# Kernel tuning notes

Hardware: AMD Instinct MI355X
Metric: run time of the kernel (lower is better)

The kernel has to match this reference:

```python
import jax, jax.numpy as jnp
import numpy as np
from jax import lax

B, L, LQ, D_IN, ET, H, INIT_EMBED = 16, 256, 64, 32, 128, 4, 8
DIM = 2 * D_IN          # attention value/feature dim (x concat mask)
ETK = ET // H           # per-head time-embedding dim


def _lin(key, fan_in, shape):
    b = 1.0 / np.sqrt(fan_in)
    return jax.random.uniform(key, shape, jnp.float32, -b, b)


def setup_inputs() -> dict:
    key = jax.random.key(0)
    ks = jax.random.split(key, 24)
    inp = {
        "x": jax.random.normal(ks[0], (B, L, D_IN), jnp.float32),
        "time_steps": jnp.sort(jax.random.uniform(ks[1], (B, L), jnp.float32), axis=-1),
        "mask": (jax.random.uniform(ks[2], (B, L, D_IN)) > 0.5).astype(jnp.float32),
        "query": jnp.linspace(0.0, 1.0, LQ, dtype=jnp.float32),
        # time embedding: Linear(1,1) and Linear(1, ET-1)
        "w_lin": _lin(ks[3], 1, (1,)), "b_lin": _lin(ks[4], 1, (1,)),
        "w_per": _lin(ks[5], 1, (ET - 1,)), "b_per": _lin(ks[6], 1, (ET - 1,)),
        # attention projections (stored as (in,out))
        "Wq": _lin(ks[7], ET, (ET, ET)), "bq": _lin(ks[8], ET, (ET,)),
        "Wk": _lin(ks[9], ET, (ET, ET)), "bk": _lin(ks[10], ET, (ET,)),
        "Wo": _lin(ks[11], H * DIM, (H * DIM, ET)), "bo": _lin(ks[12], H * DIM, (ET,)),
        # vanilla RNN (tanh)
        "W_ih": _lin(ks[13], ET, (ET, ET)), "b_ih": _lin(ks[14], ET, (ET,)),
        "W_hh": _lin(ks[15], ET, (ET, ET)), "b_hh": _lin(ks[16], ET, (ET,)),
        "r1_w": _lin(ks[17], ET, (ET, 128)), "r1_b": _lin(ks[17], ET, (128,)),
        "r2_w": _lin(ks[18], 128, (128, 128)), "r2_b": _lin(ks[18], 128, (128,)),
        "r3_w": _lin(ks[19], 128, (128, ET)), "r3_b": _lin(ks[19], 128, (ET,)),
        "r4_w": _lin(ks[20], ET, (ET, INIT_EMBED)), "r4_b": _lin(ks[20], ET, (INIT_EMBED,)),
    }
    return inp


def reference(x, time_steps, mask, query,
              w_lin, b_lin, w_per, b_per,
              Wq, bq, Wk, bk, Wo, bo,
              W_ih, b_ih, W_hh, b_hh,
              r1_w, r1_b, r2_w, r2_b, r3_w, r3_b, r4_w, r4_b):
    def time_embed(tt):  # (...,) -> (..., ET)
        tt = tt[..., None]
        return jnp.concatenate([tt * w_lin + b_lin,
                                jnp.sin(tt * w_per + b_per)], axis=-1)

    xc = jnp.concatenate([x, mask], axis=-1)          # (B,L,DIM) value
    m2 = jnp.concatenate([mask, mask], axis=-1)       # (B,L,DIM)

    kemb = time_embed(time_steps)                     # (B,L,ET)
    qemb = time_embed(query)                          # (LQ,ET)

    q = (qemb @ Wq + bq).reshape(LQ, H, ETK).transpose(1, 0, 2)       # (H,LQ,ETK)
    k = (kemb @ Wk + bk).reshape(B, L, H, ETK).transpose(0, 2, 1, 3)  # (B,H,L,ETK)

    scores = jnp.einsum('hqe,bhke->bhqk', q, k) / np.sqrt(ETK)        # (B,H,LQ,L)
    # per-feature mask broadcast: (B,H,LQ,L,DIM)
    s5 = jnp.where(m2[:, None, None, :, :] == 0, -1e9, scores[..., None])
    p = jax.nn.softmax(s5, axis=-2)                   # softmax over keys L
    att = jnp.einsum('bhqkd,bkd->bhqd', p, xc)        # (B,H,LQ,DIM)
    att = att.transpose(0, 2, 1, 3).reshape(B, LQ, H * DIM)
    out = att @ Wo + bo                               # (B,LQ,ET)

    # vanilla tanh RNN, return final hidden state
    def step(h, xt):
        h = jnp.tanh(xt @ W_ih + b_ih + h @ W_hh + b_hh)
        return h, None
    h0 = jnp.zeros((B, ET), out.dtype)
    hT, _ = lax.scan(step, h0, out.transpose(1, 0, 2))  # scan over LQ

    y = hT @ r1_w + r1_b
    y = y @ r2_w + r2_b
    y = y @ r3_w + r3_b
    y = y @ r4_w + r4_b                               # (B, INIT_EMBED)
    return y
```

## Files before the change

### kernel.cpp

```cpp
#include <hip/hip_runtime.h>
#include <hip/hip_bf16.h>


#define NB 16
#define NL 256
#define NLQ 64
#define NDIN 32
#define NET 128
#define NH 4
#define NETK 32

#define HPAD 136
#define PAD(i) ((i) + 4 * ((i) >> 6))

#define ESS 20
#define ORP 132

__global__ __launch_bounds__(128) void k_embed_proj(
    const float* __restrict__ ts, const float* __restrict__ query,
    const float* __restrict__ w_lin, const float* __restrict__ b_lin,
    const float* __restrict__ w_per, const float* __restrict__ b_per,
    const float* __restrict__ Wk, const float* __restrict__ bk,
    const float* __restrict__ Wq, const float* __restrict__ bq,
    float* __restrict__ kproj, float* __restrict__ qproj) {
  __shared__ float emb[8 * NET];
  int g = blockIdx.x;
  int j = threadIdx.x;
  bool isQ = (g >= 512);
  int base = (isQ ? g - 512 : g) * 8;
  float wl_ = w_lin[0], bl_ = b_lin[0];
  float wp = (j > 0) ? w_per[j - 1] : 0.f;
  float bp = (j > 0) ? b_per[j - 1] : 0.f;
#pragma unroll
  for (int rr = 0; rr < 8; rr++) {
    float t = isQ ? query[base + rr] : ts[base + rr];
    emb[rr * NET + j] = (j == 0) ? (t * wl_ + bl_) : sinf(t * wp + bp);
  }
  __syncthreads();
  const float* W = isQ ? Wq : Wk;
  float bias = isQ ? bq[j] : bk[j];
  float acc[8];
#pragma unroll
  for (int rr = 0; rr < 8; rr++) acc[rr] = bias;
#pragma unroll 4
  for (int i = 0; i < NET; i++) {
    float wv = W[i * NET + j];
#pragma unroll
    for (int rr = 0; rr < 8; rr++) acc[rr] += emb[rr * NET + i] * wv;
  }
  float* dst = isQ ? qproj : kproj;
#pragma unroll
  for (int rr = 0; rr < 8; rr++) dst[(size_t)(base + rr) * NET + j] = acc[rr];
}

__global__ __launch_bounds__(256) void k_attn_fused(
    const float* __restrict__ x, const float* __restrict__ mask,
    const float* __restrict__ qproj, const float* __restrict__ kproj,
    const float* __restrict__ Wo, const float* __restrict__ bo,
    const float* __restrict__ Wih, const float* __restrict__ bih,
    const float* __restrict__ bhh, float* __restrict__ XW) {
  const float SC = 0.17677669529663687f;
  int blk = blockIdx.x;
  int qg = blk & 15;
  int b  = blk >> 4;
  int t  = threadIdx.x;

  __shared__ float xs[NL * NDIN];
  __shared__ unsigned mb[NL];
  __shared__ float es[NL * ESS];
  __shared__ float qs[4 * NET];
  __shared__ float arow[4 * 256];
  __shared__ float orow[4 * ORP];

  {
    int qq = t >> 7;
    int e  = t & 127;
    qs[qq * NET + e]       = qproj[(size_t)(qg * 4 + qq) * NET + e];
    qs[(qq + 2) * NET + e] = qproj[(size_t)(qg * 4 + qq + 2) * NET + e];
  }
  {
    const float4* src = (const float4*)(x + (size_t)b * NL * NDIN);
    float4* dst = (float4*)xs;
#pragma unroll
    for (int u = 0; u < 8; u++) dst[t + 256 * u] = src[t + 256 * u];
  }
  {
    const float4* mr4 = (const float4*)(mask + (size_t)(b * NL + t) * NDIN);
    unsigned bits = 0;
#pragma unroll
    for (int u = 0; u < 8; u++) {
      float4 m = mr4[u];
      bits |= (m.x != 0.f ? 1u : 0u) << (4 * u);
      bits |= (m.y != 0.f ? 1u : 0u) << (4 * u + 1);
      bits |= (m.z != 0.f ? 1u : 0u) << (4 * u + 2);
      bits |= (m.w != 0.f ? 1u : 0u) << (4 * u + 3);
    }
    mb[t] = bits;
  }
  __syncthreads();

  for (int h = 0; h < NH; h++) {
    float kr[NETK];
    const float4* kp =
        (const float4*)(kproj + (size_t)(b * NL + t) * NET + h * NETK);
#pragma unroll
    for (int i = 0; i < 8; i++) {
      float4 v = kp[i];
      kr[4 * i] = v.x; kr[4 * i + 1] = v.y;
      kr[4 * i + 2] = v.z; kr[4 * i + 3] = v.w;
    }
#pragma unroll
    for (int qq = 0; qq < 4; qq++) {
      const float* qv = &qs[qq * NET + h * NETK];
      float s0 = 0.f, s1 = 0.f;
#pragma unroll
      for (int i = 0; i < NETK; i += 2) {
        s0 += qv[i] * kr[i];
        s1 += qv[i + 1] * kr[i + 1];
      }
      es[t * ESS + qq * 4 + h] = __expf((s0 + s1) * SC);
    }
  }
  __syncthreads();

  {
    int s = t & 1;
    int p = t >> 1;
    int qq = p >> 5;
    int c  = p & 31;
    int k0 = s * 128;
    float den[NH] = {0.f, 0.f, 0.f, 0.f};
    float num[NH] = {0.f, 0.f, 0.f, 0.f};
    float sumx = 0.f;
#pragma unroll 4
    for (int k = k0; k < k0 + 128; k++) {
      float xv = xs[k * NDIN + c];
      float mv = ((mb[k] >> c) & 1u) ? 1.f : 0.f;
      float4 e4 = *(const float4*)(es + k * ESS + qq * 4);
      sumx += xv;
      float e0 = e4.x * mv, e1 = e4.y * mv, e2 = e4.z * mv, e3 = e4.w * mv;
      den[0] += e0; num[0] += e0 * xv;
      den[1] += e1; num[1] += e1 * xv;
      den[2] += e2; num[2] += e2 * xv;
      den[3] += e3; num[3] += e3 * xv;
    }
    sumx += __shfl_xor(sumx, 1, 64);
#pragma unroll
    for (int h = 0; h < NH; h++) {
      den[h] += __shfl_xor(den[h], 1, 64);
      num[h] += __shfl_xor(num[h], 1, 64);
    }
    if (s == 0) {
      float meanx = sumx * (1.f / 256.f);
#pragma unroll
      for (int h = 0; h < NH; h++) {
        bool any = (den[h] > 0.f);
        arow[qq * 256 + h * 64 + c]      = any ? (num[h] / den[h]) : meanx;
        arow[qq * 256 + h * 64 + 32 + c] = any ? 1.f : 0.f;
      }
    }
  }
  __syncthreads();

  {
    int j = t & 127;
    int half = t >> 7;
    float o0 = bo[j], o1 = o0;
#pragma unroll 4
    for (int u = 0; u < 256; u++) {
      float w = Wo[(size_t)u * NET + j];
      o0 += arow[half * 256 + u] * w;
      o1 += arow[(half + 2) * 256 + u] * w;
    }
    orow[half * ORP + j] = o0;
    orow[(half + 2) * ORP + j] = o1;
  }
  __syncthreads();

  {
    int j = t & 127;
    int half = t >> 7;
    float a0 = bih[j] + bhh[j], a1 = a0;
#pragma unroll 4
    for (int e = 0; e < NET; e++) {
      float w = Wih[(size_t)e * NET + j];
      a0 += orow[half * ORP + e] * w;
      a1 += orow[(half + 2) * ORP + e] * w;
    }
    int q0 = qg * 4 + half;
    XW[(size_t)(b * NLQ + q0) * NET + j]     = a0;
    XW[(size_t)(b * NLQ + q0 + 2) * NET + j] = a1;
  }
}

__device__ __forceinline__ void layer128(const float* src_lds,
                                         const float* __restrict__ W,
                                         const float* __restrict__ bvec,
                                         float* dst_lds, int j, int s) {
  const float4* h4 = (const float4*)(src_lds + s * 68);
  float a0 = 0.f, a1 = 0.f, a2 = 0.f, a3 = 0.f;
#pragma unroll
  for (int i = 0; i < 16; i++) {
    float4 hv = h4[i];
    int base = (s * 64 + 4 * i) * NET + j;
    a0 += hv.x * W[base];
    a1 += hv.y * W[base + NET];
    a2 += hv.z * W[base + 2 * NET];
    a3 += hv.w * W[base + 3 * NET];
  }
  float acc = (a0 + a1) + (a2 + a3);
  acc += __shfl_xor(acc, 1, 64);
  if (s == 0) dst_lds[PAD(j)] = acc + bvec[j];
}

__global__ __launch_bounds__(256, 1) void k_rnn(
    const float* __restrict__ XW, const float* __restrict__ Whh,
    const float* __restrict__ r1w, const float* __restrict__ r1b,
    const float* __restrict__ r2w, const float* __restrict__ r2b,
    const float* __restrict__ r3w, const float* __restrict__ r3b,
    const float* __restrict__ r4w, const float* __restrict__ r4b,
    float* __restrict__ out) {
  int b = blockIdx.x;
  int tid = threadIdx.x;
  int s = tid & 1;
  int j = tid >> 1;
  __shared__ float xwl[NLQ * NET];
  __shared__ float hb[2][HPAD];
  __shared__ float tmp[HPAD];

  {
    const float4* src = (const float4*)(XW + (size_t)b * NLQ * NET);
    float4* dst = (float4*)xwl;
#pragma unroll
    for (int u = 0; u < 8; u++) dst[tid + 256 * u] = src[tid + 256 * u];
  }
  float w[64];
#pragma unroll
  for (int i = 0; i < 64; i++) w[i] = Whh[(s * 64 + i) * NET + j];

  if (tid < 128) hb[0][PAD(tid)] = 0.f;
  __syncthreads();

  for (int t = 0; t < NLQ; t++) {
    float xwv = xwl[t * NET + j];
    const float4* h4 = (const float4*)&hb[t & 1][s * 68];
    float a0 = 0.f, a1 = 0.f, a2 = 0.f, a3 = 0.f;
#pragma unroll
    for (int i = 0; i < 16; i++) {
      float4 hv = h4[i];
      a0 += hv.x * w[4 * i];
      a1 += hv.y * w[4 * i + 1];
      a2 += hv.z * w[4 * i + 2];
      a3 += hv.w * w[4 * i + 3];
    }
    float acc = (a0 + a1) + (a2 + a3);
    acc += __shfl_xor(acc, 1, 64);
    if (s == 0) {
      float z = acc + xwv;
      float e2 = __expf(2.f * z);
      hb[(t + 1) & 1][PAD(j)] = 1.f - 2.f / (e2 + 1.f);
    }
    __syncthreads();
  }

  layer128(hb[0], r1w, r1b, tmp, j, s);
  __syncthreads();
  layer128(tmp, r2w, r2b, hb[1], j, s);
  __syncthreads();
  layer128(hb[1], r3w, r3b, hb[0], j, s);
  __syncthreads();
  if (tid < 64) {
    int jj = tid >> 3, p = tid & 7;
    float y = 0.f;
#pragma unroll
    for (int i = 0; i < 16; i++) {
      int ii = p * 16 + i;
      y += hb[0][PAD(ii)] * r4w[ii * 8 + jj];
    }
    y += __shfl_xor(y, 1, 64);
    y += __shfl_xor(y, 2, 64);
    y += __shfl_xor(y, 4, 64);
    if (p == 0) out[b * 8 + jj] = y + r4b[jj];
  }
}

extern "C" void kernel_launch(void* const* d_in, const int* in_sizes, int n_in,
                              void* d_out, int out_size, void* d_ws, size_t ws_size,
                              hipStream_t stream) {
  const float* x     = (const float*)d_in[0];
  const float* ts    = (const float*)d_in[1];
  const float* mask  = (const float*)d_in[2];
  const float* query = (const float*)d_in[3];
  const float* w_lin = (const float*)d_in[4];
  const float* b_lin = (const float*)d_in[5];
  const float* w_per = (const float*)d_in[6];
  const float* b_per = (const float*)d_in[7];
  const float* Wq    = (const float*)d_in[8];
  const float* bq    = (const float*)d_in[9];
  const float* Wk    = (const float*)d_in[10];
  const float* bk    = (const float*)d_in[11];
  const float* Wo    = (const float*)d_in[12];
  const float* bo    = (const float*)d_in[13];
  const float* Wih   = (const float*)d_in[14];
  const float* bih   = (const float*)d_in[15];
  const float* Whh   = (const float*)d_in[16];
  const float* bhh   = (const float*)d_in[17];
  const float* r1w   = (const float*)d_in[18];
  const float* r1b   = (const float*)d_in[19];
  const float* r2w   = (const float*)d_in[20];
  const float* r2b   = (const float*)d_in[21];
  const float* r3w   = (const float*)d_in[22];
  const float* r3b   = (const float*)d_in[23];
  const float* r4w   = (const float*)d_in[24];
  const float* r4b   = (const float*)d_in[25];
  float* out = (float*)d_out;

  float* ws    = (float*)d_ws;
  float* kproj = ws;
  float* qproj = ws + 524288;
  float* XW    = ws + 532480;

  k_embed_proj<<<520, 128, 0, stream>>>(
      ts, query, w_lin, b_lin, w_per, b_per, Wk, bk, Wq, bq, kproj, qproj);
  k_attn_fused<<<NB * 16, 256, 0, stream>>>(
      x, mask, qproj, kproj, Wo, bo, Wih, bih, bhh, XW);
  k_rnn<<<NB, 256, 0, stream>>>(XW, Whh, r1w, r1b, r2w, r2b, r3w, r3b,
                                r4w, r4b, out);
}
```

Baseline: 195.2 us.

## Double attention block to 512 threads with split-key reduction and rotated score layout

The fused attention kernel now runs 512 threads per block instead of 256. Each thread computes scores for two heads of one key, reading q straight from global memory rather than staging it in LDS. The weighted-sum pass is split across two key halves with a partial-sum exchange through LDS. Score storage uses a rotated column layout to reduce LDS bank conflicts, and the Wo/Wih projections are given one query row per thread. This adds parallelism and more threads in flight, at the cost of extra barriers and higher register pressure from the 64-element key array.

```diff
diff --git a/kernel.cpp b/kernel.cpp
--- a/kernel.cpp
+++ b/kernel.cpp
@@ -53,7 +53,7 @@
   for (int rr = 0; rr < 8; rr++) dst[(size_t)(base + rr) * NET + j] = acc[rr];
 }
 
-__global__ __launch_bounds__(256) void k_attn_fused(
+__global__ __launch_bounds__(512, 2) void k_attn_fused(
     const float* __restrict__ x, const float* __restrict__ mask,
     const float* __restrict__ qproj, const float* __restrict__ kproj,
     const float* __restrict__ Wo, const float* __restrict__ bo,
@@ -65,26 +65,20 @@
   int b  = blk >> 4;
   int t  = threadIdx.x;
 
-  __shared__ float xs[NL * NDIN];
+  __shared__ __align__(16) float xs[NL * NDIN];
   __shared__ unsigned mb[NL];
-  __shared__ float es[NL * ESS];
-  __shared__ float qs[4 * NET];
+  __shared__ __align__(16) float es[NL * ESS];
   __shared__ float arow[4 * 256];
   __shared__ float orow[4 * ORP];
-
-  {
-    int qq = t >> 7;
-    int e  = t & 127;
-    qs[qq * NET + e]       = qproj[(size_t)(qg * 4 + qq) * NET + e];
-    qs[(qq + 2) * NET + e] = qproj[(size_t)(qg * 4 + qq + 2) * NET + e];
-  }
+  float* part = es;
+
   {
     const float4* src = (const float4*)(x + (size_t)b * NL * NDIN);
     float4* dst = (float4*)xs;
 #pragma unroll
-    for (int u = 0; u < 8; u++) dst[t + 256 * u] = src[t + 256 * u];
-  }
-  {
+    for (int u = 0; u < 4; u++) dst[t + 512 * u] = src[t + 512 * u];
+  }
+  if (t < NL) {
     const float4* mr4 = (const float4*)(mask + (size_t)(b * NL + t) * NDIN);
     unsigned bits = 0;
 #pragma unroll
@@ -99,44 +93,52 @@
   }
   __syncthreads();
 
-  for (int h = 0; h < NH; h++) {
-    float kr[NETK];
+  {
+    int k  = t & 255;
+    int hp = t >> 8;
+    float kr[64];
     const float4* kp =
-        (const float4*)(kproj + (size_t)(b * NL + t) * NET + h * NETK);
-#pragma unroll
-    for (int i = 0; i < 8; i++) {
+        (const float4*)(kproj + (size_t)(b * NL + k) * NET + hp * 64);
+#pragma unroll
+    for (int i = 0; i < 16; i++) {
       float4 v = kp[i];
       kr[4 * i] = v.x; kr[4 * i + 1] = v.y;
       kr[4 * i + 2] = v.z; kr[4 * i + 3] = v.w;
     }
+    int rot = (k >> 3) & 3;
 #pragma unroll
     for (int qq = 0; qq < 4; qq++) {
-      const float* qv = &qs[qq * NET + h * NETK];
+      const float* qrow = qproj + (size_t)(qg * 4 + qq) * NET + hp * 64;
       float s0 = 0.f, s1 = 0.f;
 #pragma unroll
-      for (int i = 0; i < NETK; i += 2) {
-        s0 += qv[i] * kr[i];
-        s1 += qv[i + 1] * kr[i + 1];
+      for (int i = 0; i < 32; i++) {
+        s0 += qrow[i] * kr[i];
+        s1 += qrow[32 + i] * kr[32 + i];
       }
-      es[t * ESS + qq * 4 + h] = __expf((s0 + s1) * SC);
-    }
-  }
-  __syncthreads();
-
-  {
-    int s = t & 1;
-    int p = t >> 1;
-    int qq = p >> 5;
-    int c  = p & 31;
-    int k0 = s * 128;
-    float den[NH] = {0.f, 0.f, 0.f, 0.f};
-    float num[NH] = {0.f, 0.f, 0.f, 0.f};
-    float sumx = 0.f;
+      float2 ev = make_float2(__expf(s0 * SC), __expf(s1 * SC));
+      int col = ((qq + rot) & 3) * 4 + hp * 2;
+      *(float2*)&es[k * ESS + col] = ev;
+    }
+  }
+  __syncthreads();
+
+  float den[NH], num[NH], sumx;
+  int qq, c, s, kh;
+  {
+    int w = t >> 6, lane = t & 63;
+    qq = w & 3; kh = w >> 2;
+    s = lane & 1; c = lane >> 1;
+    int k0 = kh * 128 + s * 64;
+#pragma unroll
+    for (int h = 0; h < NH; h++) { den[h] = 0.f; num[h] = 0.f; }
+    sumx = 0.f;
 #pragma unroll 4
-    for (int k = k0; k < k0 + 128; k++) {
+    for (int kk = 0; kk < 64; kk++) {
+      int k = k0 + kk;
       float xv = xs[k * NDIN + c];
       float mv = ((mb[k] >> c) & 1u) ? 1.f : 0.f;
-      float4 e4 = *(const float4*)(es + k * ESS + qq * 4);
+      int col = ((qq + ((k >> 3) & 3)) & 3) * 4;
+      float4 e4 = *(const float4*)(es + k * ESS + col);
       sumx += xv;
       float e0 = e4.x * mv, e1 = e4.y * mv, e2 = e4.z * mv, e3 = e4.w * mv;
       den[0] += e0; num[0] += e0 * xv;
@@ -150,46 +152,50 @@
       den[h] += __shfl_xor(den[h], 1, 64);
       num[h] += __shfl_xor(num[h], 1, 64);
     }
-    if (s == 0) {
-      float meanx = sumx * (1.f / 256.f);
-#pragma unroll
-      for (int h = 0; h < NH; h++) {
-        bool any = (den[h] > 0.f);
-        arow[qq * 256 + h * 64 + c]      = any ? (num[h] / den[h]) : meanx;
-        arow[qq * 256 + h * 64 + 32 + c] = any ? 1.f : 0.f;
-      }
+  }
+  __syncthreads();
+
+  if (kh == 1 && s == 0) {
+    float* p = part + (qq * 32 + c) * 9;
+#pragma unroll
+    for (int h = 0; h < NH; h++) { p[h] = den[h]; p[4 + h] = num[h]; }
+    p[8] = sumx;
+  }
+  __syncthreads();
+
+  if (kh == 0 && s == 0) {
+    const float* p = part + (qq * 32 + c) * 9;
+    float sx = sumx + p[8];
+    float meanx = sx * (1.f / 256.f);
+#pragma unroll
+    for (int h = 0; h < NH; h++) {
+      float d = den[h] + p[h];
+      float n = num[h] + p[4 + h];
+      bool any = (d > 0.f);
+      arow[qq * 256 + h * 64 + c]      = any ? (n / d) : meanx;
+      arow[qq * 256 + h * 64 + 32 + c] = any ? 1.f : 0.f;
     }
   }
   __syncthreads();
 
   {
     int j = t & 127;
-    int half = t >> 7;
-    float o0 = bo[j], o1 = o0;
+    int q4 = t >> 7;
+    float o = bo[j];
 #pragma unroll 4
-    for (int u = 0; u < 256; u++) {
-      float w = Wo[(size_t)u * NET + j];
-      o0 += arow[half * 256 + u] * w;
-      o1 += arow[(half + 2) * 256 + u] * w;
-    }
-    orow[half * ORP + j] = o0;
-    orow[(half + 2) * ORP + j] = o1;
+    for (int u = 0; u < 256; u++) o += arow[q4 * 256 + u] * Wo[(size_t)u * NET + j];
+    orow[q4 * ORP + j] = o;
   }
   __syncthreads();
 
   {
     int j = t & 127;
-    int half = t >> 7;
-    float a0 = bih[j] + bhh[j], a1 = a0;
+    int q4 = t >> 7;
+    float a = bih[j] + bhh[j];
 #pragma unroll 4
-    for (int e = 0; e < NET; e++) {
-      float w = Wih[(size_t)e * NET + j];
-      a0 += orow[half * ORP + e] * w;
-      a1 += orow[(half + 2) * ORP + e] * w;
-    }
-    int q0 = qg * 4 + half;
-    XW[(size_t)(b * NLQ + q0) * NET + j]     = a0;
-    XW[(size_t)(b * NLQ + q0 + 2) * NET + j] = a1;
+    for (int e = 0; e < NET; e++) a += orow[q4 * ORP + e] * Wih[(size_t)e * NET + j];
+    int q = qg * 4 + q4;
+    XW[(size_t)(b * NLQ + q) * NET + j] = a;
   }
 }
 
@@ -322,7 +328,7 @@
 
   k_embed_proj<<<520, 128, 0, stream>>>(
       ts, query, w_lin, b_lin, w_per, b_per, Wk, bk, Wq, bq, kproj, qproj);
-  k_attn_fused<<<NB * 16, 256, 0, stream>>>(
+  k_attn_fused<<<NB * 16, 512, 0, stream>>>(
       x, mask, qproj, kproj, Wo, bo, Wih, bih, bhh, XW);
   k_rnn<<<NB, 256, 0, stream>>>(XW, Whh, r1w, r1b, r2w, r2b, r3w, r3b,
                                 r4w, r4b, out);
```

Measured after the change: 198.6 us. Within noise of the previous version (+1.8%).
